# Kernel tuning notes

Hardware: AMD Instinct MI355X
Metric: run time of the kernel (lower is better)

## Reference

```python
import jax, jax.numpy as jnp
import numpy as np

RX = 49
R = 1.0
ANGLES = [-10.0, 0.0, 10.0]


def _make_kernels(rx, r, angles_deg):
    # same construction as the torch __init__
    angles = np.rad2deg(np.arctan(r * np.tan(np.deg2rad(np.asarray(angles_deg, np.float64)))))
    ks = []
    for A in angles:
        lval = np.arange(rx) - rx // 2
        lval = np.round(lval * np.tan(np.deg2rad(A))).astype(np.int32)
        ry = (lval.max() - lval.min()) // 2 * 2 + 1
        i, _ = np.meshgrid(np.arange(ry), np.arange(rx))
        i = i - ry // 2
        k = (i == lval[:, None]).astype(np.float32)[None, None]  # [1,1,rx,ry], one nonzero per row
        ks.append(k)
    return ks

_KERNELS = [jnp.asarray(k) for k in _make_kernels(RX, R, ANGLES)]
_PADS = [(int(k.shape[2]) // 2, int(k.shape[3]) // 2) for k in _KERNELS]  # (pc, pr)


def _boxfilter(x, k, pc, pr):
    # torch.conv2d(F.pad(x,(pr,pr,pc,pc)), k) == cross-correlation with symmetric zero pad
    return jax.lax.conv_general_dilated(x, k, (1, 1), ((pc, pc), (pr, pr)),
                                        dimension_numbers=('NCHW', 'OIHW', 'NCHW'))


def _reflect(x, size):
    # PyTorch reflection padding for align_corners=True: reflect about [0, size-1]
    span = size - 1
    if span <= 0:
        return jnp.zeros_like(x)
    ax = jnp.abs(x)
    extra = jnp.mod(ax, span)
    flips = jnp.floor(ax / span)
    out = jnp.where(jnp.mod(flips, 2.0) == 0.0, extra, span - extra)
    return jnp.clip(out, 0.0, span)


def _grid_sample(x, grid):
    # bilinear, padding_mode='reflection', align_corners=True; x:[B,C,H,W], grid:[B,Hg,Wg,2]
    B, C, H, W = x.shape
    gx = _reflect((grid[..., 0] + 1.0) * 0.5 * (W - 1), W)
    gy = _reflect((grid[..., 1] + 1.0) * 0.5 * (H - 1), H)
    x0 = jnp.floor(gx)
    y0 = jnp.floor(gy)
    wx = gx - x0
    wy = gy - y0
    xi0 = jnp.clip(x0, 0, W - 1).astype(jnp.int32)
    yi0 = jnp.clip(y0, 0, H - 1).astype(jnp.int32)
    xi1 = jnp.clip(x0 + 1.0, 0, W - 1).astype(jnp.int32)
    yi1 = jnp.clip(y0 + 1.0, 0, H - 1).astype(jnp.int32)
    gather = jax.vmap(lambda img, yi, xi: img[:, yi, xi])  # [B,C,Hg,Wg]
    v00 = gather(x, yi0, xi0)
    v01 = gather(x, yi0, xi1)
    v10 = gather(x, yi1, xi0)
    v11 = gather(x, yi1, xi1)
    wx = wx[:, None]  # [B,1,Hg,Wg] broadcast over channel
    wy = wy[:, None]
    return (v00 * (1 - wx) * (1 - wy) + v01 * wx * (1 - wy)
            + v10 * (1 - wx) * wy + v11 * wx * wy)


def setup_inputs() -> dict:
    key = jax.random.key(0)
    k1, k2, k3, k4 = jax.random.split(key, 4)
    B, H, W = 1, 2048, 2048
    X = jax.random.uniform(k1, (B, 1, H, W), jnp.float32)
    y = jax.random.uniform(k2, (B, 1, H, W), jnp.float32)
    hX = jax.random.normal(k3, (B, 1, H, W), jnp.float32)
    coor = jax.random.uniform(k4, (B, H, W, 2), jnp.float32, minval=-1.0, maxval=1.0)
    return {"X": X, "y": y, "hX": hX, "coor": coor}


def reference(X, y, hX, coor):
    # N: normalization = boxfilter of ones (computed once per shape in torch; recomputed here)
    N = [_boxfilter(jnp.ones_like(X), k, pc, pr) for k, (pc, pr) in zip(_KERNELS, _PADS)]
    X0 = X
    Xc = X
    for (k, (pc, pr)), Ni in zip(zip(_KERNELS, _PADS), N):
        b = _boxfilter(y - Xc, k, pc, pr) / Ni
        b = _boxfilter(b, k, pc, pr) / Ni
        Xc = Xc + b
    return _grid_sample(Xc - X0, coor) + hX
```

## Files before the change

### kernel.cpp

```cpp
#include <hip/hip_runtime.h>
#include <hip/hip_fp16.h>

static constexpr int HH = 2048;
static constexpr int WW = 2048;
static constexpr int PADT = 24;
static constexpr int PADL = 8;
static constexpr int SW   = WW + 2 * PADL;
static constexpr int PROWS = HH + 2 * PADT;
static constexpr size_t PadElems = (size_t)PROWS * SW;
static constexpr int RSP = 16;
static constexpr int RV = 16;

static constexpr float QINV = 63.5f;
static constexpr float QSC  = 2.0f / 127.0f;

__device__ constexpr int CS[9] = {-24,-19,-14,-8,-2, 3, 9,15,20};
__device__ constexpr int CE[9] = {-20,-15, -9,-3, 2, 8,14,19,24};
__device__ constexpr int CO[9] = { -4, -3, -2,-1, 0, 1, 2, 3, 4};

union U32H2 { unsigned u; __half2 h; };
__device__ __forceinline__ __half2 u2h(unsigned u) { U32H2 x; x.u = u; return x.h; }
__device__ __forceinline__ unsigned h2u(__half2 h) { U32H2 x; x.h = h; return x.u; }

__device__ __forceinline__ void swz_f(int& bx, int& by) {
  const int bid = blockIdx.x;
  const int xcd = bid & 7, i = bid >> 3;
  by = xcd * 16 + (i & 15);
  bx = i >> 4;
}

template<int SS, int EE, int OO, int NROWS>
__device__ __forceinline__ void seg2p(const __half* __restrict__ tp, int h0, int w2,
                                      __half2* __restrict__ acc) {
  constexpr int NR = EE - SS;
  constexpr bool EVEN = ((OO & 1) == 0);
  const size_t st = SW / 2;
  const unsigned* p = (const unsigned*)(tp + (size_t)(h0 + SS + PADT) * SW +
                                        (w2 + PADL + (EVEN ? OO : OO - 1)));
  unsigned ring[NR];
  __half2 s = u2h(0u);
#pragma unroll
  for (int k = 0; k < NR; ++k) {
    unsigned u;
    if constexpr (EVEN) { u = p[k * st]; }
    else { const unsigned ul = p[k * st], ur = p[k * st + 1]; u = (ul >> 16) | (ur << 16); }
    ring[k] = u;
    s = __hadd2(s, u2h(u));
  }
#pragma unroll
  for (int r = 0; r < NROWS; ++r) {
    unsigned u;
    if constexpr (EVEN) { u = p[(NR + r) * st]; }
    else { const unsigned ul = p[(NR + r) * st], ur = p[(NR + r) * st + 1]; u = (ul >> 16) | (ur << 16); }
    const __half2 v = u2h(u);
    acc[r] = __hadd2(acc[r], __hadd2(s, v));
    s = __hadd2(s, __hsub2(v, u2h(ring[r % NR])));
    ring[r % NR] = u;
  }
}

template<int SGN, int NROWS>
__device__ __forceinline__ void filt_slant2p(const __half* __restrict__ tp, int h0, int w2,
                                             __half2* __restrict__ acc) {
#pragma unroll
  for (int r = 0; r < NROWS; ++r) acc[r] = u2h(0u);
  seg2p<-24, -20, -4 * SGN, NROWS>(tp, h0, w2, acc);
  seg2p<-19, -15, -3 * SGN, NROWS>(tp, h0, w2, acc);
  seg2p<-14,  -9, -2 * SGN, NROWS>(tp, h0, w2, acc);
  seg2p< -8,  -3, -1 * SGN, NROWS>(tp, h0, w2, acc);
  seg2p< -2,   2,  0      , NROWS>(tp, h0, w2, acc);
  seg2p<  3,   8,  1 * SGN, NROWS>(tp, h0, w2, acc);
  seg2p<  9,  14,  2 * SGN, NROWS>(tp, h0, w2, acc);
  seg2p< 15,  19,  3 * SGN, NROWS>(tp, h0, w2, acc);
  seg2p< 20,  24,  4 * SGN, NROWS>(tp, h0, w2, acc);
}

template<int A>
__device__ __forceinline__ float rcpcnt(int h, int w) {
  if (h >= 24 && h <= 2023 && w >= 4 && w <= 2043) return 1.0f / 49.0f;
  int cnt = 0;
  const int sgn = (A == 0) ? -1 : 1;
#pragma unroll
  for (int j = 0; j < 9; ++j) {
    const int ww = w + sgn * CO[j];
    const int ov = min(h + CE[j], HH - 1) - max(h + CS[j], 0) + 1;
    if (ww >= 0 && ww < WW && ov > 0) cnt += ov;
  }
  return 1.0f / (float)cnt;
}

__device__ __forceinline__ float rcpcnt1(int h) {
  return 1.0f / (float)(min(h + 24, HH - 1) - max(h - 24, 0) + 1);
}

template<int A>
__global__ __launch_bounds__(256) void passA(const __half* __restrict__ tcur,
                                             __half* __restrict__ bp) {
  int bx, by; swz_f(bx, by);
  const int w2 = (bx * 256 + threadIdx.x) * 2;
  const int h0 = by * RSP;
  __half2 acc[RSP];
  filt_slant2p<(A == 0) ? -1 : 1, RSP>(tcur, h0, w2, acc);
#pragma unroll
  for (int r = 0; r < RSP; ++r) {
    const int h = h0 + r;
    const float2 f = __half22float2(acc[r]);
    *(unsigned*)(bp + (size_t)(h + PADT) * SW + (w2 + PADL)) =
        h2u(__floats2half2_rn(f.x * rcpcnt<A>(h, w2), f.y * rcpcnt<A>(h, w2 + 1)));
  }
}

template<int A>
__global__ __launch_bounds__(256) void passB(const __half* __restrict__ bp,
                                             __half* __restrict__ tcur) {
  int bx, by; swz_f(bx, by);
  const int w2 = (bx * 256 + threadIdx.x) * 2;
  const int h0 = by * RSP;
  __half2 acc[RSP];
  filt_slant2p<(A == 0) ? -1 : 1, RSP>(bp, h0, w2, acc);
#pragma unroll
  for (int r = 0; r < RSP; ++r) {
    const int h = h0 + r;
    unsigned* o = (unsigned*)(tcur + (size_t)(h + PADT) * SW + (w2 + PADL));
    const float2 cur = __half22float2(u2h(*o));
    const float2 f = __half22float2(acc[r]);
    *o = h2u(__floats2half2_rn(cur.x - f.x * rcpcnt<A>(h, w2),
                               cur.y - f.y * rcpcnt<A>(h, w2 + 1)));
  }
}

template<int A>
__global__ __launch_bounds__(256) void passBFq(const __half* __restrict__ bp,
                                               const __half* __restrict__ tcur,
                                               const __half* __restrict__ t0h,
                                               unsigned long long* __restrict__ V8) {
  int bx, by; swz_f(bx, by);
  const int w2 = (bx * 256 + threadIdx.x) * 2;
  const int h0 = by * RSP;
  __half2 acc[RSP];
  filt_slant2p<(A == 0) ? -1 : 1, RSP>(bp, h0, w2, acc);
  unsigned long long q[2][2] = {{0ull, 0ull}, {0ull, 0ull}};
#pragma unroll
  for (int r = 0; r < RSP; ++r) {
    const int h = h0 + r;
    const float2 t0 = __half22float2(u2h(*(const unsigned*)(t0h + (size_t)h * WW + w2)));
    const float2 cur = __half22float2(
        u2h(*(const unsigned*)(tcur + (size_t)(h + PADT) * SW + (w2 + PADL))));
    const float2 f = __half22float2(acc[r]);
    const float rx = t0.x - cur.x + f.x * rcpcnt<A>(h, w2);
    const float ry = t0.y - cur.y + f.y * rcpcnt<A>(h, w2 + 1);
    const int qa = min(max((int)rintf(rx * QINV), -127), 127);
    const int qb = min(max((int)rintf(ry * QINV), -127), 127);
    q[r >> 3][0] |= (unsigned long long)(unsigned char)(qa & 0xff) << ((r & 7) * 8);
    q[r >> 3][1] |= (unsigned long long)(unsigned char)(qb & 0xff) << ((r & 7) * 8);
  }
  const int c = w2 >> 1;
  ulonglong2* V16 = (ulonglong2*)V8;
  ulonglong2 o0; o0.x = q[0][0]; o0.y = q[0][1];
  ulonglong2 o1; o1.x = q[1][0]; o1.y = q[1][1];
  V16[(size_t)(h0 >> 3) * 1024 + c] = o0;
  V16[(size_t)((h0 >> 3) + 1) * 1024 + c] = o1;
}

__global__ __launch_bounds__(256) void passA1v(const __half* __restrict__ tcur,
                                               __half* __restrict__ bp) {
  int bx, by; swz_f(bx, by);
  const int w2 = (bx * 256 + threadIdx.x) * 2;
  const int h0 = by * RV;
  const size_t st = SW / 2;
  const unsigned* p = (const unsigned*)(tcur + (size_t)(h0 - 24 + PADT) * SW + (w2 + PADL));
  __half2 s = u2h(0u);
#pragma unroll
  for (int k = 0; k < 48; ++k) s = __hadd2(s, u2h(p[k * st]));
#pragma unroll
  for (int r = 0; r < RV; ++r) {
    const int h = h0 + r;
    const __half2 vin = u2h(p[(48 + r) * st]);
    const float2 f = __half22float2(__hadd2(s, vin));
    const float rc = rcpcnt1(h);
    *(unsigned*)(bp + (size_t)(h + PADT) * SW + (w2 + PADL)) =
        h2u(__floats2half2_rn(f.x * rc, f.y * rc));
    s = __hadd2(s, __hsub2(vin, u2h(p[r * st])));
  }
}

__global__ __launch_bounds__(256) void passB1v(const __half* __restrict__ bp,
                                               __half* __restrict__ tcur) {
  int bx, by; swz_f(bx, by);
  const int w2 = (bx * 256 + threadIdx.x) * 2;
  const int h0 = by * RV;
  const size_t st = SW / 2;
  const unsigned* p = (const unsigned*)(bp + (size_t)(h0 - 24 + PADT) * SW + (w2 + PADL));
  __half2 s = u2h(0u);
#pragma unroll
  for (int k = 0; k < 48; ++k) s = __hadd2(s, u2h(p[k * st]));
#pragma unroll
  for (int r = 0; r < RV; ++r) {
    const int h = h0 + r;
    const __half2 vin = u2h(p[(48 + r) * st]);
    const float2 f = __half22float2(__hadd2(s, vin));
    const float rc = rcpcnt1(h);
    unsigned* o = (unsigned*)(tcur + (size_t)(h + PADT) * SW + (w2 + PADL));
    const float2 cur = __half22float2(u2h(*o));
    *o = h2u(__floats2half2_rn(cur.x - f.x * rc, cur.y - f.y * rc));
    s = __hadd2(s, __hsub2(vin, u2h(p[r * st])));
  }
}

__global__ __launch_bounds__(256) void initk(const float* __restrict__ y,
                                             const float* __restrict__ X,
                                             __half* __restrict__ tcur,
                                             __half* __restrict__ t0h,
                                             __half* __restrict__ bp) {
  const int b = blockIdx.x;
  if (b < 4096) {
    const int i = b * 256 + threadIdx.x;
    const int p = i * 4;
    const int h = p >> 11, w = p & (WW - 1);
    const float4 Y = ((const float4*)y)[i];
    const float4 Xv = ((const float4*)X)[i];
    union { __half2 h2; unsigned u; } a, c;
    a.h2 = __floats2half2_rn(Y.x - Xv.x, Y.y - Xv.y);
    c.h2 = __floats2half2_rn(Y.z - Xv.z, Y.w - Xv.w);
    uint2 o; o.x = a.u; o.y = c.u;
    *(uint2*)(tcur + (size_t)(h + PADT) * SW + (w + PADL)) = o;
    *(uint2*)(t0h + (size_t)p) = o;
  } else {
    const int row = b - 4096;
    __half* rt = tcur + (size_t)row * SW;
    __half* rb = bp + (size_t)row * SW;
    const __half z = __float2half(0.0f);
    if (row < PADT || row >= PADT + HH) {
      for (int c = threadIdx.x; c < SW; c += 256) { rt[c] = z; rb[c] = z; }
    } else if (threadIdx.x < 2 * PADL) {
      const int c = (threadIdx.x < PADL) ? threadIdx.x : (PADL + WW + threadIdx.x - PADL);
      rt[c] = z; rb[c] = z;
    }
  }
}

__global__ __launch_bounds__(256) void gather_k(const unsigned long long* __restrict__ V8,
                                                const unsigned long long* __restrict__ coorU,
                                                const float* __restrict__ hX,
                                                float* __restrict__ out) {
  const int i = blockIdx.x * 256 + threadIdx.x;
  const unsigned long long cu = __builtin_nontemporal_load(&coorU[i]);
  union { unsigned long long u; float f[2]; } cc; cc.u = cu;
  const float gx = fminf(fmaxf((cc.f[0] + 1.0f) * 0.5f * (float)(WW - 1), 0.0f), (float)(WW - 1));
  const float gy = fminf(fmaxf((cc.f[1] + 1.0f) * 0.5f * (float)(HH - 1), 0.0f), (float)(HH - 1));
  const float x0 = floorf(gx), y0 = floorf(gy);
  const float wx = gx - x0, wy = gy - y0;
  const int xi0 = min(max((int)x0, 0), WW - 1);
  const int xi1 = min(xi0 + 1, WW - 1);
  const int yi0 = min(max((int)y0, 0), HH - 1);
  const int yi1 = min(yi0 + 1, HH - 1);
  const int s0 = yi0 >> 3, s1 = yi1 >> 3;
  const int j0 = (yi0 & 7) * 8, j1 = (yi1 & 7) * 8;
  const unsigned long long c00 = V8[(size_t)s0 * WW + xi0];
  const unsigned long long c01 = V8[(size_t)s0 * WW + xi1];
  unsigned long long c10 = c00, c11 = c01;
  if (s1 != s0) {
    c10 = V8[(size_t)s1 * WW + xi0];
    c11 = V8[(size_t)s1 * WW + xi1];
  }
  const float v00 = (float)(signed char)(c00 >> j0);
  const float v01 = (float)(signed char)(c01 >> j0);
  const float v10 = (float)(signed char)(c10 >> j1);
  const float v11 = (float)(signed char)(c11 >> j1);
  const float hx = __builtin_nontemporal_load(&hX[i]);
  const float bil = v00 * (1.0f - wx) * (1.0f - wy) + v01 * wx * (1.0f - wy) +
                    v10 * (1.0f - wx) * wy + v11 * wx * wy;
  __builtin_nontemporal_store(bil * QSC + hx, &out[i]);
}

extern "C" void kernel_launch(void* const* d_in, const int* in_sizes, int n_in,
                              void* d_out, int out_size, void* d_ws, size_t ws_size,
                              hipStream_t stream) {
  const float* X    = (const float*)d_in[0];
  const float* y    = (const float*)d_in[1];
  const float* hX   = (const float*)d_in[2];
  const float* coor = (const float*)d_in[3];
  float* out = (float*)d_out;

  __half* tcur = (__half*)d_ws;
  __half* bp   = tcur + PadElems;
  __half* t0h  = bp + PadElems;
  unsigned long long* V8 = (unsigned long long*)(t0h + (size_t)HH * WW);

  const int n = HH * WW;
  const int fblocks = (WW / 512) * (HH / RSP);

  initk<<<4096 + PROWS, 256, 0, stream>>>(y, X, tcur, t0h, bp);

  passA<0><<<fblocks, 256, 0, stream>>>(tcur, bp);
  passB<0><<<fblocks, 256, 0, stream>>>(bp, tcur);
  passA1v<<<fblocks, 256, 0, stream>>>(tcur, bp);
  passB1v<<<fblocks, 256, 0, stream>>>(bp, tcur);
  passA<2><<<fblocks, 256, 0, stream>>>(tcur, bp);
  passBFq<2><<<fblocks, 256, 0, stream>>>(bp, tcur, t0h, V8);

  gather_k<<<n / 256, 256, 0, stream>>>(V8, (const unsigned long long*)coor, hX, out);
}
```

Before: 139.7 us.

## Stage slanted filter input tiles in shared memory with smaller row strips

The slanted-filter passes now copy a (8+48)-row by 524-column halo tile into LDS before filtering, and read all taps from shared memory instead of global memory. Rows per block drop from 16 to 8, which doubles the block count and changes the block swizzle, and the quantized output is packed as one 8-row word per block. The aim is to cut repeated global and L2 traffic from overlapping slanted taps. The cost is more halo overhead per output row, since 56 rows are staged for 8 outputs, plus an LDS footprint of about 58KB per block that limits occupancy.

Result: slower. 157.1 us (+12.4%).

```diff
diff --git a/kernel.cpp b/kernel.cpp
--- a/kernel.cpp
+++ b/kernel.cpp
@@ -8,8 +8,11 @@
 static constexpr int SW   = WW + 2 * PADL;
 static constexpr int PROWS = HH + 2 * PADT;
 static constexpr size_t PadElems = (size_t)PROWS * SW;
-static constexpr int RSP = 16;
+static constexpr int RSP = 8;
 static constexpr int RV = 16;
+static constexpr int TR = RSP + 48;
+static constexpr int TC = 524;
+static constexpr int TCd = TC / 2;
 
 static constexpr float QINV = 63.5f;
 static constexpr float QSC  = 2.0f / 127.0f;
@@ -22,6 +25,12 @@
 __device__ __forceinline__ __half2 u2h(unsigned u) { U32H2 x; x.u = u; return x.h; }
 __device__ __forceinline__ unsigned h2u(__half2 h) { U32H2 x; x.h = h; return x.u; }
 
+__device__ __forceinline__ void swz_s(int& bx, int& by) {
+  const int bid = blockIdx.x;
+  const int xcd = bid & 7, i = bid >> 3;
+  by = xcd * 32 + (i & 31);
+  bx = i >> 5;
+}
 __device__ __forceinline__ void swz_f(int& bx, int& by) {
   const int bid = blockIdx.x;
   const int xcd = bid & 7, i = bid >> 3;
@@ -29,29 +38,41 @@
   bx = i >> 4;
 }
 
-template<int SS, int EE, int OO, int NROWS>
-__device__ __forceinline__ void seg2p(const __half* __restrict__ tp, int h0, int w2,
+__device__ __forceinline__ void stage_tile(const __half* __restrict__ src, int h0, int bx,
+                                           __half* __restrict__ tile) {
+  const int wv = threadIdx.x >> 6, ln = threadIdx.x & 63;
+  for (int j = 0; j < TR / 4; ++j) {
+    const int lr = wv * (TR / 4) + j;
+    const uint2* srow = (const uint2*)(src + (size_t)(h0 + lr) * SW) + (bx * 128 + 1);
+    uint2* drow = (uint2*)(tile + (size_t)lr * TC);
+    drow[ln] = srow[ln];
+    drow[ln + 64] = srow[ln + 64];
+    if (ln < 3) drow[ln + 128] = srow[ln + 128];
+  }
+}
+
+template<int SS, int EE, int OO>
+__device__ __forceinline__ void seg2l(const __half* __restrict__ tile, int w2l,
                                       __half2* __restrict__ acc) {
   constexpr int NR = EE - SS;
   constexpr bool EVEN = ((OO & 1) == 0);
-  const size_t st = SW / 2;
-  const unsigned* p = (const unsigned*)(tp + (size_t)(h0 + SS + PADT) * SW +
-                                        (w2 + PADL + (EVEN ? OO : OO - 1)));
+  const unsigned* p = (const unsigned*)tile + (size_t)(SS + 24) * TCd +
+                      ((w2l + 4 + (EVEN ? OO : OO - 1)) >> 1);
   unsigned ring[NR];
   __half2 s = u2h(0u);
 #pragma unroll
   for (int k = 0; k < NR; ++k) {
     unsigned u;
-    if constexpr (EVEN) { u = p[k * st]; }
-    else { const unsigned ul = p[k * st], ur = p[k * st + 1]; u = (ul >> 16) | (ur << 16); }
+    if constexpr (EVEN) { u = p[k * TCd]; }
+    else { const unsigned ul = p[k * TCd], ur = p[k * TCd + 1]; u = (ul >> 16) | (ur << 16); }
     ring[k] = u;
     s = __hadd2(s, u2h(u));
   }
 #pragma unroll
-  for (int r = 0; r < NROWS; ++r) {
+  for (int r = 0; r < RSP; ++r) {
     unsigned u;
-    if constexpr (EVEN) { u = p[(NR + r) * st]; }
-    else { const unsigned ul = p[(NR + r) * st], ur = p[(NR + r) * st + 1]; u = (ul >> 16) | (ur << 16); }
+    if constexpr (EVEN) { u = p[(NR + r) * TCd]; }
+    else { const unsigned ul = p[(NR + r) * TCd], ur = p[(NR + r) * TCd + 1]; u = (ul >> 16) | (ur << 16); }
     const __half2 v = u2h(u);
     acc[r] = __hadd2(acc[r], __hadd2(s, v));
     s = __hadd2(s, __hsub2(v, u2h(ring[r % NR])));
@@ -59,20 +80,20 @@
   }
 }
 
-template<int SGN, int NROWS>
-__device__ __forceinline__ void filt_slant2p(const __half* __restrict__ tp, int h0, int w2,
+template<int SGN>
+__device__ __forceinline__ void filt_slant2l(const __half* __restrict__ tile, int w2l,
                                              __half2* __restrict__ acc) {
 #pragma unroll
-  for (int r = 0; r < NROWS; ++r) acc[r] = u2h(0u);
-  seg2p<-24, -20, -4 * SGN, NROWS>(tp, h0, w2, acc);
-  seg2p<-19, -15, -3 * SGN, NROWS>(tp, h0, w2, acc);
-  seg2p<-14,  -9, -2 * SGN, NROWS>(tp, h0, w2, acc);
-  seg2p< -8,  -3, -1 * SGN, NROWS>(tp, h0, w2, acc);
-  seg2p< -2,   2,  0      , NROWS>(tp, h0, w2, acc);
-  seg2p<  3,   8,  1 * SGN, NROWS>(tp, h0, w2, acc);
-  seg2p<  9,  14,  2 * SGN, NROWS>(tp, h0, w2, acc);
-  seg2p< 15,  19,  3 * SGN, NROWS>(tp, h0, w2, acc);
-  seg2p< 20,  24,  4 * SGN, NROWS>(tp, h0, w2, acc);
+  for (int r = 0; r < RSP; ++r) acc[r] = u2h(0u);
+  seg2l<-24, -20, -4 * SGN>(tile, w2l, acc);
+  seg2l<-19, -15, -3 * SGN>(tile, w2l, acc);
+  seg2l<-14,  -9, -2 * SGN>(tile, w2l, acc);
+  seg2l< -8,  -3, -1 * SGN>(tile, w2l, acc);
+  seg2l< -2,   2,  0      >(tile, w2l, acc);
+  seg2l<  3,   8,  1 * SGN>(tile, w2l, acc);
+  seg2l<  9,  14,  2 * SGN>(tile, w2l, acc);
+  seg2l< 15,  19,  3 * SGN>(tile, w2l, acc);
+  seg2l< 20,  24,  4 * SGN>(tile, w2l, acc);
 }
 
 template<int A>
@@ -94,13 +115,17 @@
 }
 
 template<int A>
-__global__ __launch_bounds__(256) void passA(const __half* __restrict__ tcur,
-                                             __half* __restrict__ bp) {
-  int bx, by; swz_f(bx, by);
-  const int w2 = (bx * 256 + threadIdx.x) * 2;
+__global__ __launch_bounds__(256) void passA_l(const __half* __restrict__ tcur,
+                                               __half* __restrict__ bp) {
+  __shared__ __half tile[TR * TC];
+  int bx, by; swz_s(bx, by);
+  const int w2l = 2 * threadIdx.x;
+  const int w2 = bx * 512 + w2l;
   const int h0 = by * RSP;
+  stage_tile(tcur, h0, bx, tile);
+  __syncthreads();
   __half2 acc[RSP];
-  filt_slant2p<(A == 0) ? -1 : 1, RSP>(tcur, h0, w2, acc);
+  filt_slant2l<(A == 0) ? -1 : 1>(tile, w2l, acc);
 #pragma unroll
   for (int r = 0; r < RSP; ++r) {
     const int h = h0 + r;
@@ -111,13 +136,17 @@
 }
 
 template<int A>
-__global__ __launch_bounds__(256) void passB(const __half* __restrict__ bp,
-                                             __half* __restrict__ tcur) {
-  int bx, by; swz_f(bx, by);
-  const int w2 = (bx * 256 + threadIdx.x) * 2;
+__global__ __launch_bounds__(256) void passB_l(const __half* __restrict__ bp,
+                                               __half* __restrict__ tcur) {
+  __shared__ __half tile[TR * TC];
+  int bx, by; swz_s(bx, by);
+  const int w2l = 2 * threadIdx.x;
+  const int w2 = bx * 512 + w2l;
   const int h0 = by * RSP;
+  stage_tile(bp, h0, bx, tile);
+  __syncthreads();
   __half2 acc[RSP];
-  filt_slant2p<(A == 0) ? -1 : 1, RSP>(bp, h0, w2, acc);
+  filt_slant2l<(A == 0) ? -1 : 1>(tile, w2l, acc);
 #pragma unroll
   for (int r = 0; r < RSP; ++r) {
     const int h = h0 + r;
@@ -130,16 +159,20 @@
 }
 
 template<int A>
-__global__ __launch_bounds__(256) void passBFq(const __half* __restrict__ bp,
-                                               const __half* __restrict__ tcur,
-                                               const __half* __restrict__ t0h,
-                                               unsigned long long* __restrict__ V8) {
-  int bx, by; swz_f(bx, by);
-  const int w2 = (bx * 256 + threadIdx.x) * 2;
+__global__ __launch_bounds__(256) void passBFq_l(const __half* __restrict__ bp,
+                                                 const __half* __restrict__ tcur,
+                                                 const __half* __restrict__ t0h,
+                                                 unsigned long long* __restrict__ V8) {
+  __shared__ __half tile[TR * TC];
+  int bx, by; swz_s(bx, by);
+  const int w2l = 2 * threadIdx.x;
+  const int w2 = bx * 512 + w2l;
   const int h0 = by * RSP;
+  stage_tile(bp, h0, bx, tile);
+  __syncthreads();
   __half2 acc[RSP];
-  filt_slant2p<(A == 0) ? -1 : 1, RSP>(bp, h0, w2, acc);
-  unsigned long long q[2][2] = {{0ull, 0ull}, {0ull, 0ull}};
+  filt_slant2l<(A == 0) ? -1 : 1>(tile, w2l, acc);
+  unsigned long long qa = 0ull, qb = 0ull;
 #pragma unroll
   for (int r = 0; r < RSP; ++r) {
     const int h = h0 + r;
@@ -149,17 +182,14 @@
     const float2 f = __half22float2(acc[r]);
     const float rx = t0.x - cur.x + f.x * rcpcnt<A>(h, w2);
     const float ry = t0.y - cur.y + f.y * rcpcnt<A>(h, w2 + 1);
-    const int qa = min(max((int)rintf(rx * QINV), -127), 127);
-    const int qb = min(max((int)rintf(ry * QINV), -127), 127);
-    q[r >> 3][0] |= (unsigned long long)(unsigned char)(qa & 0xff) << ((r & 7) * 8);
-    q[r >> 3][1] |= (unsigned long long)(unsigned char)(qb & 0xff) << ((r & 7) * 8);
-  }
-  const int c = w2 >> 1;
+    const int ia = min(max((int)rintf(rx * QINV), -127), 127);
+    const int ib = min(max((int)rintf(ry * QINV), -127), 127);
+    qa |= (unsigned long long)(unsigned char)(ia & 0xff) << (r * 8);
+    qb |= (unsigned long long)(unsigned char)(ib & 0xff) << (r * 8);
+  }
   ulonglong2* V16 = (ulonglong2*)V8;
-  ulonglong2 o0; o0.x = q[0][0]; o0.y = q[0][1];
-  ulonglong2 o1; o1.x = q[1][0]; o1.y = q[1][1];
-  V16[(size_t)(h0 >> 3) * 1024 + c] = o0;
-  V16[(size_t)((h0 >> 3) + 1) * 1024 + c] = o1;
+  ulonglong2 o; o.x = qa; o.y = qb;
+  V16[(size_t)(h0 >> 3) * 1024 + (w2 >> 1)] = o;
 }
 
 __global__ __launch_bounds__(256) void passA1v(const __half* __restrict__ tcur,
@@ -288,16 +318,17 @@
   unsigned long long* V8 = (unsigned long long*)(t0h + (size_t)HH * WW);
 
   const int n = HH * WW;
-  const int fblocks = (WW / 512) * (HH / RSP);
+  const int sblocks = (WW / 512) * (HH / RSP);
+  const int vblocks = (WW / 512) * (HH / RV);
 
   initk<<<4096 + PROWS, 256, 0, stream>>>(y, X, tcur, t0h, bp);
 
-  passA<0><<<fblocks, 256, 0, stream>>>(tcur, bp);
-  passB<0><<<fblocks, 256, 0, stream>>>(bp, tcur);
-  passA1v<<<fblocks, 256, 0, stream>>>(tcur, bp);
-  passB1v<<<fblocks, 256, 0, stream>>>(bp, tcur);
-  passA<2><<<fblocks, 256, 0, stream>>>(tcur, bp);
-  passBFq<2><<<fblocks, 256, 0, stream>>>(bp, tcur, t0h, V8);
+  passA_l<0><<<sblocks, 256, 0, stream>>>(tcur, bp);
+  passB_l<0><<<sblocks, 256, 0, stream>>>(bp, tcur);
+  passA1v<<<vblocks, 256, 0, stream>>>(tcur, bp);
+  passB1v<<<vblocks, 256, 0, stream>>>(bp, tcur);
+  passA_l<2><<<sblocks, 256, 0, stream>>>(tcur, bp);
+  passBFq_l<2><<<sblocks, 256, 0, stream>>>(bp, tcur, t0h, V8);
 
   gather_k<<<n / 256, 256, 0, stream>>>(V8, (const unsigned long long*)coor, hX, out);
 }
```
